# Kernel optimization log

Measured on AMD Instinct MI355X. Metric: run time of the kernel, lower is better.

Reference implementation:

```python
import jax, jax.numpy as jnp
import numpy as np
import math

BATCH, DIM, T, WIDTH = 4096, 100, 101, 200

def setup_inputs() -> dict:
    key = jax.random.key(0)
    ks = jax.random.split(key, 12)
    def lin(k, nin, nout):
        bound = 1.0 / math.sqrt(nin)
        kw, kb = jax.random.split(k)
        W = jax.random.uniform(kw, (nin, nout), jnp.float32, -bound, bound)
        b = jax.random.uniform(kb, (nout,), jnp.float32, -bound, bound)
        return W, b
    W0, b0 = lin(ks[0], DIM + 1, WIDTH)
    W1, b1 = lin(ks[1], WIDTH, WIDTH)
    W2, b2 = lin(ks[2], WIDTH, WIDTH)
    W3, b3 = lin(ks[3], WIDTH, WIDTH)
    Wout, bout = lin(ks[4], WIDTH, DIM)
    S0 = jax.random.normal(ks[5], (BATCH, DIM), jnp.float32)
    # standard-normal increments; scaled by sqrt(h) inside reference (matches torch randn * sqrt(h))
    dW = jax.random.normal(ks[6], (BATCH, DIM * T), jnp.float32)
    timegrid = jnp.linspace(0.0, 1.0, T, dtype=jnp.float32)
    return {"S0": S0, "timegrid": timegrid, "dW": dW,
            "W0": W0, "b0": b0, "W1": W1, "b1": b1, "W2": W2, "b2": b2,
            "W3": W3, "b3": b3, "Wout": Wout, "bout": bout}

def _mlp(x, W0, b0, W1, b1, W2, b2, W3, b3, Wout, bout):
    h = jax.nn.relu(x @ W0 + b0)
    h = jax.nn.relu(h @ W1 + b1)
    h = jax.nn.relu(h @ W2 + b2)
    h = jax.nn.relu(h @ W3 + b3)
    return h @ Wout + bout

def reference(S0, timegrid, dW, W0, b0, W1, b1, W2, b2, W3, b3, Wout, bout):
    B, dim = S0.shape
    T_ = timegrid.shape[0]
    h = timegrid[1] - timegrid[0]
    # [B, T*dim] -> [T-1, B, dim]: slices (i-1)*dim:i*dim for i=1..T-1
    dWs = jnp.sqrt(h) * jnp.transpose(dW.reshape(B, T_, dim)[:, :T_ - 1], (1, 0, 2))
    ts = timegrid[:T_ - 1]  # t_{i-1} for i = 1..T-1

    def step(carry, xs):
        S, err = carry
        t, dWi = xs
        inp = jnp.concatenate([jnp.broadcast_to(t, (B, 1)), S], axis=1)
        u = _mlp(inp, W0, b0, W1, b1, W2, b2, W3, b3, Wout, bout)
        err = err + (u * u) * h          # ff_fun running cost
        S = S + u * h + u * dWi          # drift b_fun=u, diffusion sigma_fun=u
        return (S, err), None

    (S_final, err), _ = jax.lax.scan(step, (S0, jnp.zeros_like(S0)), (ts, dWs))
    return err + S_final * S_final       # terminal cost g_fun(x,u)=x*x
```

## Files before the change

### kernel.cpp

```cpp
#include <hip/hip_runtime.h>


typedef __attribute__((ext_vector_type(8))) short  bf16x8;
typedef __attribute__((ext_vector_type(4))) float  f32x4;

#define MFMA16(A,B,C) __builtin_amdgcn_mfma_f32_16x16x32_bf16((A),(B),(C),0,0,0)

#define FS 232

#define OFF1 26624
#define E1   46592
#define OFF2 (OFF1+E1)
#define OFF3 (OFF2+E1)
#define OFF4 (OFF3+E1)
#define TOTE (OFF4+7*7*512)

__device__ __forceinline__ unsigned short f2bf(float x){
  unsigned u = __float_as_uint(x);
  return (unsigned short)((u + 0x7fffu + ((u >> 16) & 1u)) >> 16);
}

__global__ void pack_w(const float* __restrict__ W0, const float* __restrict__ b0,
                       const float* __restrict__ W1, const float* __restrict__ b1,
                       const float* __restrict__ W2, const float* __restrict__ b2,
                       const float* __restrict__ W3, const float* __restrict__ b3,
                       const float* __restrict__ Wo, const float* __restrict__ bo,
                       unsigned short* __restrict__ out){
  int idx = blockIdx.x * 256 + threadIdx.x;
  if (idx >= TOTE) return;
  const float *Ws, *bs; int KI, NT, local, isw0 = 0;
  if      (idx < OFF1){ Ws = W0; bs = b0; KI = 4; NT = 200; local = idx;        isw0 = 1; }
  else if (idx < OFF2){ Ws = W1; bs = b1; KI = 7; NT = 200; local = idx - OFF1; }
  else if (idx < OFF3){ Ws = W2; bs = b2; KI = 7; NT = 200; local = idx - OFF2; }
  else if (idx < OFF4){ Ws = W3; bs = b3; KI = 7; NT = 200; local = idx - OFF3; }
  else                { Ws = Wo; bs = bo; KI = 7; NT = 100; local = idx - OFF4; }
  int per_tile = KI * 512;
  int tile = local / per_tile;
  int rem  = local - tile * per_tile;
  int kit  = rem >> 9;
  int within = rem & 511;
  int ln = within >> 3, j = within & 7;
  int n = tile * 16 + (ln & 15);
  int k = kit * 32 + (ln >> 4) * 8 + j;
  float v = 0.f;
  if (n < NT){
    if (isw0){
      if      (k < 100)  v = Ws[(1 + k) * 200 + n];
      else if (k == 100) v = Ws[n];
      else if (k == 101) v = bs[n];
    } else {
      if      (k < 200)  v = Ws[k * NT + n];
      else if (k == 200) v = bs[n];
    }
  }
  out[idx] = f2bf(v);
}

__global__ __launch_bounds__(512, 2) __attribute__((amdgpu_waves_per_eu(2, 2)))
void solver(const float* __restrict__ S0, const float* __restrict__ tg,
            const float* __restrict__ dW, const unsigned short* __restrict__ Wp,
            float* __restrict__ outp)
{
  __shared__ __attribute__((aligned(16))) unsigned short sW0[26624];
  __shared__ __attribute__((aligned(16))) unsigned short sIn[16 * FS];
  __shared__ __attribute__((aligned(16))) unsigned short sA [16 * FS];
  __shared__ __attribute__((aligned(16))) unsigned short sB [16 * FS];

  const int tid  = threadIdx.x;
  const int lane = tid & 63;
  const int w    = tid >> 6;
  const int q    = lane >> 4;
  const int mr   = lane & 15;
  const int blk  = blockIdx.x;
  const bool has2   = (w < 5);
  const bool hasOut = (w < 7);
  const int t0 = w, t1 = w + 8;
  const int f0 = w * 16 + q * 4;
  const bool fvalid = hasOut && (f0 <= 96);
  const int rowoff = mr * FS;

  for (int i = tid; i < 16 * FS / 2; i += 512){
    ((unsigned*)sIn)[i] = 0u; ((unsigned*)sA)[i] = 0u; ((unsigned*)sB)[i] = 0u;
  }
  for (int i = tid; i < 3328; i += 512)
    ((uint4*)sW0)[i] = ((const uint4*)Wp)[i];
  if (tid < 16){
    sIn[tid * FS + 101] = 0x3F80;
    sA [tid * FS + 200] = 0x3F80;
    sB [tid * FS + 200] = 0x3F80;
  }

  bf16x8 w1f[2][7], w2f[2][7], w3f[2][7], wo_f[7];
#pragma unroll
  for (int k = 0; k < 7; ++k){
    w1f[0][k] = *(const bf16x8*)(Wp + OFF1 + ((t0 * 7 + k) * 64 + lane) * 8);
    w2f[0][k] = *(const bf16x8*)(Wp + OFF2 + ((t0 * 7 + k) * 64 + lane) * 8);
    w3f[0][k] = *(const bf16x8*)(Wp + OFF3 + ((t0 * 7 + k) * 64 + lane) * 8);
  }
  if (has2){
#pragma unroll
    for (int k = 0; k < 7; ++k){
      w1f[1][k] = *(const bf16x8*)(Wp + OFF1 + ((t1 * 7 + k) * 64 + lane) * 8);
      w2f[1][k] = *(const bf16x8*)(Wp + OFF2 + ((t1 * 7 + k) * 64 + lane) * 8);
      w3f[1][k] = *(const bf16x8*)(Wp + OFF3 + ((t1 * 7 + k) * 64 + lane) * 8);
    }
  }
  if (hasOut){
#pragma unroll
    for (int k = 0; k < 7; ++k)
      wo_f[k] = *(const bf16x8*)(Wp + OFF4 + ((w * 7 + k) * 64 + lane) * 8);
  }

  float Sr[4] = {0.f, 0.f, 0.f, 0.f}, Er[4] = {0.f, 0.f, 0.f, 0.f};
  if (fvalid){
    f32x4 s0v = *(const f32x4*)(S0 + (blk * 16 + mr) * 100 + f0);
#pragma unroll
    for (int i = 0; i < 4; ++i) Sr[i] = s0v[i];
    unsigned lo = (unsigned)f2bf(Sr[0]) | ((unsigned)f2bf(Sr[1]) << 16);
    unsigned hi = (unsigned)f2bf(Sr[2]) | ((unsigned)f2bf(Sr[3]) << 16);
    uint2 pp; pp.x = lo; pp.y = hi;
    *(uint2*)&sIn[rowoff + f0] = pp;
  }

  const float hh = tg[1] - tg[0];
  const float sq = sqrtf(hh);
  float tcur = tg[0];

#define EPI(DST, TL, ACC) {                                                   \
    int ff = (TL) * 16 + q * 4;                                               \
    if (!((TL) == 12 && q >= 2)){                                             \
      float v0 = fmaxf((ACC)[0], 0.f), v1 = fmaxf((ACC)[1], 0.f);             \
      float v2 = fmaxf((ACC)[2], 0.f), v3 = fmaxf((ACC)[3], 0.f);             \
      unsigned lo = (unsigned)f2bf(v0) | ((unsigned)f2bf(v1) << 16);          \
      unsigned hi = (unsigned)f2bf(v2) | ((unsigned)f2bf(v3) << 16);          \
      uint2 pp; pp.x = lo; pp.y = hi;                                         \
      *(uint2*)&(DST)[rowoff + ff] = pp;                                      \
    } }

#define HIDDEN(SRC, DST, WF) {                                                \
    f32x4 acc0 = {0.f,0.f,0.f,0.f}, acc1 = {0.f,0.f,0.f,0.f};                 \
    _Pragma("unroll")                                                         \
    for (int k = 0; k < 7; ++k){                                              \
      bf16x8 b = *(const bf16x8*)((SRC) + rowoff + k * 32 + q * 8);           \
      acc0 = MFMA16(WF[0][k], b, acc0);                                       \
      if (has2) acc1 = MFMA16(WF[1][k], b, acc1);                             \
    }                                                                         \
    EPI(DST, t0, acc0)                                                        \
    if (has2) EPI(DST, t1, acc1)                                              \
  }

  __syncthreads();

  for (int t = 0; t < 100; ++t){
    f32x4 dwf = {0.f, 0.f, 0.f, 0.f};
    if (fvalid)
      dwf = *(const f32x4*)(dW + (blk * 16 + mr) * 10100 + t * 100 + f0);
    if (tid < 16) sIn[tid * FS + 100] = f2bf(tcur);
    float tnext = tg[t + 1];
    __syncthreads();

    {
      f32x4 acc0 = {0.f,0.f,0.f,0.f}, acc1 = {0.f,0.f,0.f,0.f};
#pragma unroll
      for (int k = 0; k < 4; ++k){
        bf16x8 b  = *(const bf16x8*)(sIn + rowoff + k * 32 + q * 8);
        bf16x8 a0 = *(const bf16x8*)(sW0 + ((t0 * 4 + k) * 64 + lane) * 8);
        acc0 = MFMA16(a0, b, acc0);
        if (has2){
          bf16x8 a1 = *(const bf16x8*)(sW0 + ((t1 * 4 + k) * 64 + lane) * 8);
          acc1 = MFMA16(a1, b, acc1);
        }
      }
      EPI(sA, t0, acc0)
      if (has2) EPI(sA, t1, acc1)
    }
    __syncthreads();
    HIDDEN(sA, sB, w1f)
    __syncthreads();
    HIDDEN(sB, sA, w2f)
    __syncthreads();
    HIDDEN(sA, sB, w3f)
    __syncthreads();

    if (hasOut){
      f32x4 a4 = {0.f, 0.f, 0.f, 0.f};
#pragma unroll
      for (int k = 0; k < 7; ++k){
        bf16x8 b = *(const bf16x8*)(sB + rowoff + k * 32 + q * 8);
        a4 = MFMA16(wo_f[k], b, a4);
      }
      if (fvalid){
#pragma unroll
        for (int i = 0; i < 4; ++i){
          float u = a4[i];
          Er[i] += u * u * hh;
          Sr[i] += u * (hh + sq * dwf[i]);
        }
        unsigned lo = (unsigned)f2bf(Sr[0]) | ((unsigned)f2bf(Sr[1]) << 16);
        unsigned hi = (unsigned)f2bf(Sr[2]) | ((unsigned)f2bf(Sr[3]) << 16);
        uint2 pp; pp.x = lo; pp.y = hi;
        *(uint2*)&sIn[rowoff + f0] = pp;
      }
    }
    tcur = tnext;
  }

  if (fvalid){
    f32x4 o;
#pragma unroll
    for (int i = 0; i < 4; ++i) o[i] = Er[i] + Sr[i] * Sr[i];
    *(f32x4*)(outp + (blk * 16 + mr) * 100 + f0) = o;
  }
#undef HIDDEN
#undef EPI
}

extern "C" void kernel_launch(void* const* d_in, const int* in_sizes, int n_in,
                              void* d_out, int out_size, void* d_ws, size_t ws_size,
                              hipStream_t stream) {
  const float* S0 = (const float*)d_in[0];
  const float* tg = (const float*)d_in[1];
  const float* dW = (const float*)d_in[2];
  const float* W0 = (const float*)d_in[3];
  const float* b0 = (const float*)d_in[4];
  const float* W1 = (const float*)d_in[5];
  const float* b1 = (const float*)d_in[6];
  const float* W2 = (const float*)d_in[7];
  const float* b2 = (const float*)d_in[8];
  const float* W3 = (const float*)d_in[9];
  const float* b3 = (const float*)d_in[10];
  const float* Wo = (const float*)d_in[11];
  const float* bo = (const float*)d_in[12];
  unsigned short* Wp = (unsigned short*)d_ws;

  pack_w<<<(TOTE + 255) / 256, 256, 0, stream>>>(W0, b0, W1, b1, W2, b2, W3, b3,
                                                 Wo, bo, Wp);
  solver<<<256, 512, 0, stream>>>(S0, tg, dW, Wp, (float*)d_out);
}
```

Baseline: 456.2 us.

## Use 4 waves per block with 3-4 output tiles each, tile 12 in LDS

Changes the solver from 8 waves to 4 waves per block. Each wave now owns three 16-column tiles per hidden layer, plus two tiles of the output layer, with weights kept in registers. The leftover tile 12 of each hidden layer is staged in shared memory and computed by wave 3. The aim is less barrier and sync overhead, better balance across waves and more MFMA work per wave. In exchange there is more register pressure at one wave per SIMD, less latency hiding, and wave 3 carries more work than the others. It also switches bf16 packing to a hardware pack builtin when one is available.

```diff
diff --git a/kernel.cpp b/kernel.cpp
--- a/kernel.cpp
+++ b/kernel.cpp
@@ -5,6 +5,7 @@
 typedef __attribute__((ext_vector_type(4))) float  f32x4;
 
 #define MFMA16(A,B,C) __builtin_amdgcn_mfma_f32_16x16x32_bf16((A),(B),(C),0,0,0)
+#define KEEP(x) asm volatile("" : "+v"(x))
 
 #define FS 232
 
@@ -18,6 +19,16 @@
 __device__ __forceinline__ unsigned short f2bf(float x){
   unsigned u = __float_as_uint(x);
   return (unsigned short)((u + 0x7fffu + ((u >> 16) & 1u)) >> 16);
+}
+
+__device__ __forceinline__ unsigned pk2(float a, float b){
+#if __has_builtin(__builtin_amdgcn_cvt_pk_bf16_f32)
+  typedef __bf16 bf2 __attribute__((ext_vector_type(2)));
+  bf2 r = __builtin_amdgcn_cvt_pk_bf16_f32(a, b);
+  return __builtin_bit_cast(unsigned, r);
+#else
+  return (unsigned)f2bf(a) | ((unsigned)f2bf(b) << 16);
+#endif
 }
 
 __global__ void pack_w(const float* __restrict__ W0, const float* __restrict__ b0,
@@ -56,12 +67,13 @@
   out[idx] = f2bf(v);
 }
 
-__global__ __launch_bounds__(512, 2) __attribute__((amdgpu_waves_per_eu(2, 2)))
+__global__ __launch_bounds__(256, 1) __attribute__((amdgpu_waves_per_eu(1, 1)))
 void solver(const float* __restrict__ S0, const float* __restrict__ tg,
             const float* __restrict__ dW, const unsigned short* __restrict__ Wp,
             float* __restrict__ outp)
 {
-  __shared__ __attribute__((aligned(16))) unsigned short sW0[26624];
+  __shared__ __attribute__((aligned(16))) unsigned short sW0 [26624];
+  __shared__ __attribute__((aligned(16))) unsigned short sT12[10752];
   __shared__ __attribute__((aligned(16))) unsigned short sIn[16 * FS];
   __shared__ __attribute__((aligned(16))) unsigned short sA [16 * FS];
   __shared__ __attribute__((aligned(16))) unsigned short sB [16 * FS];
@@ -72,144 +84,178 @@
   const int q    = lane >> 4;
   const int mr   = lane & 15;
   const int blk  = blockIdx.x;
-  const bool has2   = (w < 5);
-  const bool hasOut = (w < 7);
-  const int t0 = w, t1 = w + 8;
-  const int f0 = w * 16 + q * 4;
-  const bool fvalid = hasOut && (f0 <= 96);
+  const bool isw3 = (w == 3);
   const int rowoff = mr * FS;
-
-  for (int i = tid; i < 16 * FS / 2; i += 512){
+  const int row  = blk * 16 + mr;
+
+  const int f0a = w * 16 + q * 4;
+  const int f0b = (w + 4) * 16 + q * 4;
+  const bool v1ok = (w < 3) && (f0b <= 96);
+
+  for (int i = tid; i < 16 * FS / 2; i += 256){
     ((unsigned*)sIn)[i] = 0u; ((unsigned*)sA)[i] = 0u; ((unsigned*)sB)[i] = 0u;
   }
-  for (int i = tid; i < 3328; i += 512)
+  for (int i = tid; i < 3328; i += 256)
     ((uint4*)sW0)[i] = ((const uint4*)Wp)[i];
+  for (int i = tid; i < 1344; i += 256){
+    int L = i / 448;
+    ((uint4*)sT12)[i] = *(const uint4*)(Wp + OFF1 + L * E1 + 84 * 512 + (i - L * 448) * 8);
+  }
   if (tid < 16){
     sIn[tid * FS + 101] = 0x3F80;
     sA [tid * FS + 200] = 0x3F80;
     sB [tid * FS + 200] = 0x3F80;
   }
 
-  bf16x8 w1f[2][7], w2f[2][7], w3f[2][7], wo_f[7];
-#pragma unroll
-  for (int k = 0; k < 7; ++k){
-    w1f[0][k] = *(const bf16x8*)(Wp + OFF1 + ((t0 * 7 + k) * 64 + lane) * 8);
-    w2f[0][k] = *(const bf16x8*)(Wp + OFF2 + ((t0 * 7 + k) * 64 + lane) * 8);
-    w3f[0][k] = *(const bf16x8*)(Wp + OFF3 + ((t0 * 7 + k) * 64 + lane) * 8);
-  }
-  if (has2){
+  bf16x8 w1f[3][7], w2f[3][7], w3f[3][7], wo_f[2][7];
+#pragma unroll
+  for (int j = 0; j < 3; ++j){
+    int tl = w + 4 * j;
 #pragma unroll
     for (int k = 0; k < 7; ++k){
-      w1f[1][k] = *(const bf16x8*)(Wp + OFF1 + ((t1 * 7 + k) * 64 + lane) * 8);
-      w2f[1][k] = *(const bf16x8*)(Wp + OFF2 + ((t1 * 7 + k) * 64 + lane) * 8);
-      w3f[1][k] = *(const bf16x8*)(Wp + OFF3 + ((t1 * 7 + k) * 64 + lane) * 8);
-    }
-  }
-  if (hasOut){
-#pragma unroll
-    for (int k = 0; k < 7; ++k)
-      wo_f[k] = *(const bf16x8*)(Wp + OFF4 + ((w * 7 + k) * 64 + lane) * 8);
-  }
-
-  float Sr[4] = {0.f, 0.f, 0.f, 0.f}, Er[4] = {0.f, 0.f, 0.f, 0.f};
-  if (fvalid){
-    f32x4 s0v = *(const f32x4*)(S0 + (blk * 16 + mr) * 100 + f0);
-#pragma unroll
-    for (int i = 0; i < 4; ++i) Sr[i] = s0v[i];
-    unsigned lo = (unsigned)f2bf(Sr[0]) | ((unsigned)f2bf(Sr[1]) << 16);
-    unsigned hi = (unsigned)f2bf(Sr[2]) | ((unsigned)f2bf(Sr[3]) << 16);
-    uint2 pp; pp.x = lo; pp.y = hi;
-    *(uint2*)&sIn[rowoff + f0] = pp;
+      w1f[j][k] = *(const bf16x8*)(Wp + OFF1 + (tl * 7 + k) * 512 + lane * 8);
+      w2f[j][k] = *(const bf16x8*)(Wp + OFF2 + (tl * 7 + k) * 512 + lane * 8);
+      w3f[j][k] = *(const bf16x8*)(Wp + OFF3 + (tl * 7 + k) * 512 + lane * 8);
+    }
+  }
+  {
+    int ta = w, tb = (w < 3) ? (w + 4) : w;
+#pragma unroll
+    for (int k = 0; k < 7; ++k){
+      wo_f[0][k] = *(const bf16x8*)(Wp + OFF4 + (ta * 7 + k) * 512 + lane * 8);
+      wo_f[1][k] = *(const bf16x8*)(Wp + OFF4 + (tb * 7 + k) * 512 + lane * 8);
+    }
+  }
+#pragma unroll
+  for (int j = 0; j < 3; ++j)
+#pragma unroll
+    for (int k = 0; k < 7; ++k){ KEEP(w1f[j][k]); KEEP(w2f[j][k]); KEEP(w3f[j][k]); }
+#pragma unroll
+  for (int k = 0; k < 7; ++k){ KEEP(wo_f[0][k]); KEEP(wo_f[1][k]); }
+
+  float Sr0[4], Er0[4] = {0.f,0.f,0.f,0.f};
+  float Sr1[4] = {0.f,0.f,0.f,0.f}, Er1[4] = {0.f,0.f,0.f,0.f};
+  {
+    f32x4 v = *(const f32x4*)(S0 + row * 100 + f0a);
+#pragma unroll
+    for (int i = 0; i < 4; ++i) Sr0[i] = v[i];
+    uint2 pp; pp.x = pk2(Sr0[0], Sr0[1]); pp.y = pk2(Sr0[2], Sr0[3]);
+    *(uint2*)&sIn[rowoff + f0a] = pp;
+  }
+  if (v1ok){
+    f32x4 v = *(const f32x4*)(S0 + row * 100 + f0b);
+#pragma unroll
+    for (int i = 0; i < 4; ++i) Sr1[i] = v[i];
+    uint2 pp; pp.x = pk2(Sr1[0], Sr1[1]); pp.y = pk2(Sr1[2], Sr1[3]);
+    *(uint2*)&sIn[rowoff + f0b] = pp;
   }
 
   const float hh = tg[1] - tg[0];
   const float sq = sqrtf(hh);
   float tcur = tg[0];
 
-#define EPI(DST, TL, ACC) {                                                   \
-    int ff = (TL) * 16 + q * 4;                                               \
-    if (!((TL) == 12 && q >= 2)){                                             \
+#define EPI(DST, TL, ACC, T12) {                                              \
+    if (!(T12) || q < 2){                                                     \
+      int ff = (TL) * 16 + q * 4;                                             \
       float v0 = fmaxf((ACC)[0], 0.f), v1 = fmaxf((ACC)[1], 0.f);             \
       float v2 = fmaxf((ACC)[2], 0.f), v3 = fmaxf((ACC)[3], 0.f);             \
-      unsigned lo = (unsigned)f2bf(v0) | ((unsigned)f2bf(v1) << 16);          \
-      unsigned hi = (unsigned)f2bf(v2) | ((unsigned)f2bf(v3) << 16);          \
-      uint2 pp; pp.x = lo; pp.y = hi;                                         \
-      *(uint2*)&(DST)[rowoff + ff] = pp;                                      \
-    } }
-
-#define HIDDEN(SRC, DST, WF) {                                                \
-    f32x4 acc0 = {0.f,0.f,0.f,0.f}, acc1 = {0.f,0.f,0.f,0.f};                 \
+      uint2 pp; pp.x = pk2(v0, v1); pp.y = pk2(v2, v3);                       \
+      *(uint2*)&(DST)[rowoff + ff] = pp; } }
+
+#define HIDDEN(SRC, DST, WF, LIDX) {                                          \
+    f32x4 c0 = {0.f,0.f,0.f,0.f}, c1 = c0, c2 = c0, c3 = c0;                  \
     _Pragma("unroll")                                                         \
     for (int k = 0; k < 7; ++k){                                              \
       bf16x8 b = *(const bf16x8*)((SRC) + rowoff + k * 32 + q * 8);           \
-      acc0 = MFMA16(WF[0][k], b, acc0);                                       \
-      if (has2) acc1 = MFMA16(WF[1][k], b, acc1);                             \
-    }                                                                         \
-    EPI(DST, t0, acc0)                                                        \
-    if (has2) EPI(DST, t1, acc1)                                              \
-  }
-
-  __syncthreads();
+      c0 = MFMA16(WF[0][k], b, c0);                                           \
+      c1 = MFMA16(WF[1][k], b, c1);                                           \
+      c2 = MFMA16(WF[2][k], b, c2);                                           \
+      if (isw3){                                                              \
+        bf16x8 at = *(const bf16x8*)(sT12 + ((LIDX) * 7 + k) * 512 + lane * 8);\
+        c3 = MFMA16(at, b, c3); } }                                           \
+    EPI(DST, w,     c0, 0)                                                    \
+    EPI(DST, w + 4, c1, 0)                                                    \
+    EPI(DST, w + 8, c2, 0)                                                    \
+    if (isw3) EPI(DST, 12, c3, 1) }
 
   for (int t = 0; t < 100; ++t){
-    f32x4 dwf = {0.f, 0.f, 0.f, 0.f};
-    if (fvalid)
-      dwf = *(const f32x4*)(dW + (blk * 16 + mr) * 10100 + t * 100 + f0);
+    f32x4 dwf0 = {0.f,0.f,0.f,0.f}, dwf1 = {0.f,0.f,0.f,0.f};
+    dwf0 = *(const f32x4*)(dW + row * 10100 + t * 100 + f0a);
+    if (v1ok) dwf1 = *(const f32x4*)(dW + row * 10100 + t * 100 + f0b);
     if (tid < 16) sIn[tid * FS + 100] = f2bf(tcur);
     float tnext = tg[t + 1];
     __syncthreads();
 
     {
-      f32x4 acc0 = {0.f,0.f,0.f,0.f}, acc1 = {0.f,0.f,0.f,0.f};
+      f32x4 c0 = {0.f,0.f,0.f,0.f}, c1 = c0, c2 = c0, c3 = c0;
 #pragma unroll
       for (int k = 0; k < 4; ++k){
         bf16x8 b  = *(const bf16x8*)(sIn + rowoff + k * 32 + q * 8);
-        bf16x8 a0 = *(const bf16x8*)(sW0 + ((t0 * 4 + k) * 64 + lane) * 8);
-        acc0 = MFMA16(a0, b, acc0);
-        if (has2){
-          bf16x8 a1 = *(const bf16x8*)(sW0 + ((t1 * 4 + k) * 64 + lane) * 8);
-          acc1 = MFMA16(a1, b, acc1);
+        bf16x8 a0 = *(const bf16x8*)(sW0 + ((w    ) * 4 + k) * 512 + lane * 8);
+        bf16x8 a1 = *(const bf16x8*)(sW0 + ((w + 4) * 4 + k) * 512 + lane * 8);
+        bf16x8 a2 = *(const bf16x8*)(sW0 + ((w + 8) * 4 + k) * 512 + lane * 8);
+        c0 = MFMA16(a0, b, c0);
+        c1 = MFMA16(a1, b, c1);
+        c2 = MFMA16(a2, b, c2);
+        if (isw3){
+          bf16x8 a3 = *(const bf16x8*)(sW0 + (48 + k) * 512 + lane * 8);
+          c3 = MFMA16(a3, b, c3);
         }
       }
-      EPI(sA, t0, acc0)
-      if (has2) EPI(sA, t1, acc1)
-    }
-    __syncthreads();
-    HIDDEN(sA, sB, w1f)
-    __syncthreads();
-    HIDDEN(sB, sA, w2f)
-    __syncthreads();
-    HIDDEN(sA, sB, w3f)
-    __syncthreads();
-
-    if (hasOut){
-      f32x4 a4 = {0.f, 0.f, 0.f, 0.f};
+      EPI(sA, w,     c0, 0)
+      EPI(sA, w + 4, c1, 0)
+      EPI(sA, w + 8, c2, 0)
+      if (isw3) EPI(sA, 12, c3, 1)
+    }
+    __syncthreads();
+    HIDDEN(sA, sB, w1f, 0)
+    __syncthreads();
+    HIDDEN(sB, sA, w2f, 1)
+    __syncthreads();
+    HIDDEN(sA, sB, w3f, 2)
+    __syncthreads();
+
+    {
+      f32x4 u0 = {0.f,0.f,0.f,0.f}, u1 = u0;
 #pragma unroll
       for (int k = 0; k < 7; ++k){
         bf16x8 b = *(const bf16x8*)(sB + rowoff + k * 32 + q * 8);
-        a4 = MFMA16(wo_f[k], b, a4);
-      }
-      if (fvalid){
+        u0 = MFMA16(wo_f[0][k], b, u0);
+        if (w < 3) u1 = MFMA16(wo_f[1][k], b, u1);
+      }
+#pragma unroll
+      for (int i = 0; i < 4; ++i){
+        float u = u0[i];
+        Er0[i] += u * u * hh;
+        Sr0[i] += u * (hh + sq * dwf0[i]);
+      }
+      { uint2 pp; pp.x = pk2(Sr0[0], Sr0[1]); pp.y = pk2(Sr0[2], Sr0[3]);
+        *(uint2*)&sIn[rowoff + f0a] = pp; }
+      if (v1ok){
 #pragma unroll
         for (int i = 0; i < 4; ++i){
-          float u = a4[i];
-          Er[i] += u * u * hh;
-          Sr[i] += u * (hh + sq * dwf[i]);
+          float u = u1[i];
+          Er1[i] += u * u * hh;
+          Sr1[i] += u * (hh + sq * dwf1[i]);
         }
-        unsigned lo = (unsigned)f2bf(Sr[0]) | ((unsigned)f2bf(Sr[1]) << 16);
-        unsigned hi = (unsigned)f2bf(Sr[2]) | ((unsigned)f2bf(Sr[3]) << 16);
-        uint2 pp; pp.x = lo; pp.y = hi;
-        *(uint2*)&sIn[rowoff + f0] = pp;
+        uint2 pp; pp.x = pk2(Sr1[0], Sr1[1]); pp.y = pk2(Sr1[2], Sr1[3]);
+        *(uint2*)&sIn[rowoff + f0b] = pp;
       }
     }
     tcur = tnext;
   }
 
-  if (fvalid){
+  {
     f32x4 o;
 #pragma unroll
-    for (int i = 0; i < 4; ++i) o[i] = Er[i] + Sr[i] * Sr[i];
-    *(f32x4*)(outp + (blk * 16 + mr) * 100 + f0) = o;
+    for (int i = 0; i < 4; ++i) o[i] = Er0[i] + Sr0[i] * Sr0[i];
+    *(f32x4*)(outp + row * 100 + f0a) = o;
+  }
+  if (v1ok){
+    f32x4 o;
+#pragma unroll
+    for (int i = 0; i < 4; ++i) o[i] = Er1[i] + Sr1[i] * Sr1[i];
+    *(f32x4*)(outp + row * 100 + f0b) = o;
   }
 #undef HIDDEN
 #undef EPI
@@ -235,5 +281,5 @@
 
   pack_w<<<(TOTE + 255) / 256, 256, 0, stream>>>(W0, b0, W1, b1, W2, b2, W3, b3,
                                                  Wo, bo, Wp);
-  solver<<<256, 512, 0, stream>>>(S0, tg, dW, Wp, (float*)d_out);
-}
+  solver<<<256, 256, 0, stream>>>(S0, tg, dW, Wp, (float*)d_out);
+}
```

Result: slower. 593.3 us (+30.1%).

## Store activations in MFMA fragment order in LDS and pin weight registers

Applied to the files above, without the earlier changes.

Activation buffers in shared memory now use a swizzled layout that matches the MFMA B-operand fragment order, replacing the padded row-major layout with stride 232. Each lane then reads its bf16x8 operand as one contiguous (k*64+lane)*8 load, which is meant to avoid bank conflicts and address arithmetic on the latency-bound sequential time loop. Weight fragments are now loaded unconditionally, using clamped tile indices for waves that have no second or output tile, and pinned in VGPRs with empty asm constraints so the compiler cannot rematerialise or spill them. This raises register pressure and makes the epilogue's scattered 8-byte writes depend on the new slot mapping.

```diff
diff --git a/kernel.cpp b/kernel.cpp
--- a/kernel.cpp
+++ b/kernel.cpp
@@ -5,8 +5,7 @@
 typedef __attribute__((ext_vector_type(4))) float  f32x4;
 
 #define MFMA16(A,B,C) __builtin_amdgcn_mfma_f32_16x16x32_bf16((A),(B),(C),0,0,0)
-
-#define FS 232
+#define KEEP(x) asm volatile("" : "+v"(x))
 
 #define OFF1 26624
 #define E1   46592
@@ -18,6 +17,10 @@
 __device__ __forceinline__ unsigned short f2bf(float x){
   unsigned u = __float_as_uint(x);
   return (unsigned short)((u + 0x7fffu + ((u >> 16) & 1u)) >> 16);
+}
+
+__device__ __forceinline__ unsigned pk2(float a, float b){
+  return (unsigned)f2bf(a) | ((unsigned)f2bf(b) << 16);
 }
 
 __global__ void pack_w(const float* __restrict__ W0, const float* __restrict__ b0,
@@ -62,64 +65,62 @@
             float* __restrict__ outp)
 {
   __shared__ __attribute__((aligned(16))) unsigned short sW0[26624];
-  __shared__ __attribute__((aligned(16))) unsigned short sIn[16 * FS];
-  __shared__ __attribute__((aligned(16))) unsigned short sA [16 * FS];
-  __shared__ __attribute__((aligned(16))) unsigned short sB [16 * FS];
+  __shared__ __attribute__((aligned(16))) unsigned short sIn[2048];
+  __shared__ __attribute__((aligned(16))) unsigned short sA [3584];
+  __shared__ __attribute__((aligned(16))) unsigned short sB [3584];
 
   const int tid  = threadIdx.x;
   const int lane = tid & 63;
   const int w    = tid >> 6;
   const int q    = lane >> 4;
   const int mr   = lane & 15;
-  const int blk  = blockIdx.x;
+  const int row  = blockIdx.x * 16 + mr;
   const bool has2   = (w < 5);
   const bool hasOut = (w < 7);
-  const int t0 = w, t1 = w + 8;
   const int f0 = w * 16 + q * 4;
-  const bool fvalid = hasOut && (f0 <= 96);
-  const int rowoff = mr * FS;
-
-  for (int i = tid; i < 16 * FS / 2; i += 512){
-    ((unsigned*)sIn)[i] = 0u; ((unsigned*)sA)[i] = 0u; ((unsigned*)sB)[i] = 0u;
-  }
+  const bool fvalid = hasOut && !(w == 6 && q >= 1);
+
+#define FSLOT(f, m) ((((f) >> 5) * 64 + ((((f) >> 3) & 3) * 16) + (m)) * 8 + ((f) & 7))
+
   for (int i = tid; i < 3328; i += 512)
     ((uint4*)sW0)[i] = ((const uint4*)Wp)[i];
+  for (int i = tid; i < 1024; i += 512) ((unsigned*)sIn)[i] = 0u;
+  for (int i = tid; i < 1792; i += 512){ ((unsigned*)sA)[i] = 0u; ((unsigned*)sB)[i] = 0u; }
+  __syncthreads();
   if (tid < 16){
-    sIn[tid * FS + 101] = 0x3F80;
-    sA [tid * FS + 200] = 0x3F80;
-    sB [tid * FS + 200] = 0x3F80;
-  }
-
+    sIn[FSLOT(101, tid)] = 0x3F80;
+    sA [FSLOT(200, tid)] = 0x3F80;
+    sB [FSLOT(200, tid)] = 0x3F80;
+  }
+
+  const int t1  = has2   ? (w + 8) : w;
+  const int two = hasOut ? w : 0;
   bf16x8 w1f[2][7], w2f[2][7], w3f[2][7], wo_f[7];
 #pragma unroll
   for (int k = 0; k < 7; ++k){
-    w1f[0][k] = *(const bf16x8*)(Wp + OFF1 + ((t0 * 7 + k) * 64 + lane) * 8);
-    w2f[0][k] = *(const bf16x8*)(Wp + OFF2 + ((t0 * 7 + k) * 64 + lane) * 8);
-    w3f[0][k] = *(const bf16x8*)(Wp + OFF3 + ((t0 * 7 + k) * 64 + lane) * 8);
-  }
-  if (has2){
-#pragma unroll
-    for (int k = 0; k < 7; ++k){
-      w1f[1][k] = *(const bf16x8*)(Wp + OFF1 + ((t1 * 7 + k) * 64 + lane) * 8);
-      w2f[1][k] = *(const bf16x8*)(Wp + OFF2 + ((t1 * 7 + k) * 64 + lane) * 8);
-      w3f[1][k] = *(const bf16x8*)(Wp + OFF3 + ((t1 * 7 + k) * 64 + lane) * 8);
-    }
-  }
-  if (hasOut){
-#pragma unroll
-    for (int k = 0; k < 7; ++k)
-      wo_f[k] = *(const bf16x8*)(Wp + OFF4 + ((w * 7 + k) * 64 + lane) * 8);
-  }
-
-  float Sr[4] = {0.f, 0.f, 0.f, 0.f}, Er[4] = {0.f, 0.f, 0.f, 0.f};
+    w1f[0][k] = *(const bf16x8*)(Wp + OFF1 + (w  * 7 + k) * 512 + lane * 8);
+    w1f[1][k] = *(const bf16x8*)(Wp + OFF1 + (t1 * 7 + k) * 512 + lane * 8);
+    w2f[0][k] = *(const bf16x8*)(Wp + OFF2 + (w  * 7 + k) * 512 + lane * 8);
+    w2f[1][k] = *(const bf16x8*)(Wp + OFF2 + (t1 * 7 + k) * 512 + lane * 8);
+    w3f[0][k] = *(const bf16x8*)(Wp + OFF3 + (w  * 7 + k) * 512 + lane * 8);
+    w3f[1][k] = *(const bf16x8*)(Wp + OFF3 + (t1 * 7 + k) * 512 + lane * 8);
+    wo_f[k]   = *(const bf16x8*)(Wp + OFF4 + (two * 7 + k) * 512 + lane * 8);
+  }
+#pragma unroll
+  for (int k = 0; k < 7; ++k){
+    KEEP(w1f[0][k]); KEEP(w1f[1][k]);
+    KEEP(w2f[0][k]); KEEP(w2f[1][k]);
+    KEEP(w3f[0][k]); KEEP(w3f[1][k]);
+    KEEP(wo_f[k]);
+  }
+
+  float Sr[4] = {0.f,0.f,0.f,0.f}, Er[4] = {0.f,0.f,0.f,0.f};
   if (fvalid){
-    f32x4 s0v = *(const f32x4*)(S0 + (blk * 16 + mr) * 100 + f0);
-#pragma unroll
-    for (int i = 0; i < 4; ++i) Sr[i] = s0v[i];
-    unsigned lo = (unsigned)f2bf(Sr[0]) | ((unsigned)f2bf(Sr[1]) << 16);
-    unsigned hi = (unsigned)f2bf(Sr[2]) | ((unsigned)f2bf(Sr[3]) << 16);
-    uint2 pp; pp.x = lo; pp.y = hi;
-    *(uint2*)&sIn[rowoff + f0] = pp;
+    f32x4 v = *(const f32x4*)(S0 + row * 100 + f0);
+#pragma unroll
+    for (int i = 0; i < 4; ++i) Sr[i] = v[i];
+    uint2 pp; pp.x = pk2(Sr[0], Sr[1]); pp.y = pk2(Sr[2], Sr[3]);
+    *(uint2*)&sIn[FSLOT(f0, mr)] = pp;
   }
 
   const float hh = tg[1] - tg[0];
@@ -127,52 +128,47 @@
   float tcur = tg[0];
 
 #define EPI(DST, TL, ACC) {                                                   \
-    int ff = (TL) * 16 + q * 4;                                               \
     if (!((TL) == 12 && q >= 2)){                                             \
-      float v0 = fmaxf((ACC)[0], 0.f), v1 = fmaxf((ACC)[1], 0.f);             \
-      float v2 = fmaxf((ACC)[2], 0.f), v3 = fmaxf((ACC)[3], 0.f);             \
-      unsigned lo = (unsigned)f2bf(v0) | ((unsigned)f2bf(v1) << 16);          \
-      unsigned hi = (unsigned)f2bf(v2) | ((unsigned)f2bf(v3) << 16);          \
-      uint2 pp; pp.x = lo; pp.y = hi;                                         \
-      *(uint2*)&(DST)[rowoff + ff] = pp;                                      \
-    } }
+      int ff = (TL) * 16 + q * 4;                                             \
+      uint2 pp;                                                               \
+      pp.x = pk2(fmaxf((ACC)[0], 0.f), fmaxf((ACC)[1], 0.f));                 \
+      pp.y = pk2(fmaxf((ACC)[2], 0.f), fmaxf((ACC)[3], 0.f));                 \
+      *(uint2*)&(DST)[FSLOT(ff, mr)] = pp; } }
 
 #define HIDDEN(SRC, DST, WF) {                                                \
-    f32x4 acc0 = {0.f,0.f,0.f,0.f}, acc1 = {0.f,0.f,0.f,0.f};                 \
+    f32x4 c0 = {0.f,0.f,0.f,0.f}, c1 = c0;                                    \
     _Pragma("unroll")                                                         \
     for (int k = 0; k < 7; ++k){                                              \
-      bf16x8 b = *(const bf16x8*)((SRC) + rowoff + k * 32 + q * 8);           \
-      acc0 = MFMA16(WF[0][k], b, acc0);                                       \
-      if (has2) acc1 = MFMA16(WF[1][k], b, acc1);                             \
+      bf16x8 b = *(const bf16x8*)((SRC) + (k * 64 + lane) * 8);               \
+      c0 = MFMA16(WF[0][k], b, c0);                                           \
+      if (has2) c1 = MFMA16(WF[1][k], b, c1);                                 \
     }                                                                         \
-    EPI(DST, t0, acc0)                                                        \
-    if (has2) EPI(DST, t1, acc1)                                              \
-  }
-
-  __syncthreads();
+    EPI(DST, w, c0)                                                           \
+    if (has2) EPI(DST, w + 8, c1)                                             \
+  }
 
   for (int t = 0; t < 100; ++t){
-    f32x4 dwf = {0.f, 0.f, 0.f, 0.f};
+    f32x4 dwf = {0.f,0.f,0.f,0.f};
     if (fvalid)
-      dwf = *(const f32x4*)(dW + (blk * 16 + mr) * 10100 + t * 100 + f0);
-    if (tid < 16) sIn[tid * FS + 100] = f2bf(tcur);
+      dwf = *(const f32x4*)(dW + row * 10100 + t * 100 + f0);
+    if (tid < 16) sIn[FSLOT(100, tid)] = f2bf(tcur);
     float tnext = tg[t + 1];
     __syncthreads();
 
     {
-      f32x4 acc0 = {0.f,0.f,0.f,0.f}, acc1 = {0.f,0.f,0.f,0.f};
+      f32x4 c0 = {0.f,0.f,0.f,0.f}, c1 = c0;
 #pragma unroll
       for (int k = 0; k < 4; ++k){
-        bf16x8 b  = *(const bf16x8*)(sIn + rowoff + k * 32 + q * 8);
-        bf16x8 a0 = *(const bf16x8*)(sW0 + ((t0 * 4 + k) * 64 + lane) * 8);
-        acc0 = MFMA16(a0, b, acc0);
+        bf16x8 b  = *(const bf16x8*)(sIn + (k * 64 + lane) * 8);
+        bf16x8 a0 = *(const bf16x8*)(sW0 + (w * 4 + k) * 512 + lane * 8);
+        c0 = MFMA16(a0, b, c0);
         if (has2){
-          bf16x8 a1 = *(const bf16x8*)(sW0 + ((t1 * 4 + k) * 64 + lane) * 8);
-          acc1 = MFMA16(a1, b, acc1);
+          bf16x8 a1 = *(const bf16x8*)(sW0 + ((w + 8) * 4 + k) * 512 + lane * 8);
+          c1 = MFMA16(a1, b, c1);
         }
       }
-      EPI(sA, t0, acc0)
-      if (has2) EPI(sA, t1, acc1)
+      EPI(sA, w, c0)
+      if (has2) EPI(sA, w + 8, c1)
     }
     __syncthreads();
     HIDDEN(sA, sB, w1f)
@@ -183,23 +179,20 @@
     __syncthreads();
 
     if (hasOut){
-      f32x4 a4 = {0.f, 0.f, 0.f, 0.f};
+      f32x4 u = {0.f,0.f,0.f,0.f};
 #pragma unroll
       for (int k = 0; k < 7; ++k){
-        bf16x8 b = *(const bf16x8*)(sB + rowoff + k * 32 + q * 8);
-        a4 = MFMA16(wo_f[k], b, a4);
+        bf16x8 b = *(const bf16x8*)(sB + (k * 64 + lane) * 8);
+        u = MFMA16(wo_f[k], b, u);
       }
       if (fvalid){
 #pragma unroll
         for (int i = 0; i < 4; ++i){
-          float u = a4[i];
-          Er[i] += u * u * hh;
-          Sr[i] += u * (hh + sq * dwf[i]);
+          Er[i] += u[i] * u[i] * hh;
+          Sr[i] += u[i] * (hh + sq * dwf[i]);
         }
-        unsigned lo = (unsigned)f2bf(Sr[0]) | ((unsigned)f2bf(Sr[1]) << 16);
-        unsigned hi = (unsigned)f2bf(Sr[2]) | ((unsigned)f2bf(Sr[3]) << 16);
-        uint2 pp; pp.x = lo; pp.y = hi;
-        *(uint2*)&sIn[rowoff + f0] = pp;
+        uint2 pp; pp.x = pk2(Sr[0], Sr[1]); pp.y = pk2(Sr[2], Sr[3]);
+        *(uint2*)&sIn[FSLOT(f0, mr)] = pp;
       }
     }
     tcur = tnext;
@@ -209,10 +202,11 @@
     f32x4 o;
 #pragma unroll
     for (int i = 0; i < 4; ++i) o[i] = Er[i] + Sr[i] * Sr[i];
-    *(f32x4*)(outp + (blk * 16 + mr) * 100 + f0) = o;
+    *(f32x4*)(outp + row * 100 + f0) = o;
   }
 #undef HIDDEN
 #undef EPI
+#undef FSLOT
 }
 
 extern "C" void kernel_launch(void* const* d_in, const int* in_sizes, int n_in,
```

New measurement: 451.8 us. Within noise of the previous version (-1.0%).
